# Optimization experiments

Hardware: AMD Instinct MI355X
Metric: run time of the kernel (lower is better)

Reference implementation:

```python
import jax, jax.numpy as jnp
import numpy as np

N = 50000
D_IN = 512
D_OUT = 512
NUM_SAMPLE = 2


def setup_inputs() -> dict:
    key = jax.random.key(0)
    ks = jax.random.split(key, 8)
    x = jax.random.normal(ks[0], (N, D_IN), dtype=jnp.float32)
    neighs1 = jax.random.randint(ks[1], (N, NUM_SAMPLE), 0, N, dtype=jnp.int32)
    neighs2 = jax.random.randint(ks[2], (N, NUM_SAMPLE), 0, N, dtype=jnp.int32)
    # SageLayer weights: [out, 2*in] (self || aggregated neighbors), xavier-ish scale
    W1 = jax.random.normal(ks[3], (D_OUT, 2 * D_IN), dtype=jnp.float32) * 0.03
    W2 = jax.random.normal(ks[4], (D_OUT, 2 * D_OUT), dtype=jnp.float32) * 0.03
    fc_w = jax.random.normal(ks[5], (2, N * D_OUT), dtype=jnp.float32) * 0.0005
    fc_b = jnp.zeros((2,), dtype=jnp.float32)
    return {"x": x, "neighs1": neighs1, "neighs2": neighs2,
            "W1": W1, "W2": W2, "fc_w": fc_w, "fc_b": fc_b}


def _sage_layer(h, neighs, W):
    # MEAN aggregation over the num_sample sampled neighbors (self excluded, gcn=False).
    # Equivalent to the original dense one-hot mask.div(num_neigh).mm(embed_matrix).
    agg = h[neighs].mean(axis=1)                      # [N, S, d] -> [N, d]
    combined = jnp.concatenate([h, agg], axis=1)      # [N, 2d]
    # F.relu(W.mm(combined.t())).t() == relu(combined @ W.T)
    return jax.nn.relu(combined @ W.T)                # [N, out]


def reference(x, neighs1, neighs2, W1, W2, fc_w, fc_b):
    h = _sage_layer(x, neighs1, W1)
    h = _sage_layer(h, neighs2, W2)
    flat = h.reshape(1, -1)                           # [1, N*out]
    logits = flat @ fc_w.T + fc_b                     # [1, 2]
    return (flat, jax.nn.log_softmax(logits, axis=1))
```

## Files before the change

### kernel.cpp

```cpp
#include <hip/hip_runtime.h>
#include <stdint.h>

typedef short bf16x8 __attribute__((ext_vector_type(8)));
typedef float f32x4 __attribute__((ext_vector_type(4)));
typedef unsigned short u16x8 __attribute__((ext_vector_type(8)));

#define N_NODES 50000
#define DIM 512
#define KDIM 1024
#define NPAD 50048
#define M_TILES 391
#define GEMM_GRID 1568
#define FLAT_TOTAL 25600000ULL
#define NBLK_AGG 12500

__device__ __forceinline__ unsigned short f2bf(float f) {
    unsigned u = __float_as_uint(f);
    unsigned r = u + 0x7FFFu + ((u >> 16) & 1u);
    return (unsigned short)(r >> 16);
}
__device__ __forceinline__ float bf2f(unsigned short h) {
    return __uint_as_float(((unsigned)h) << 16);
}

__device__ __forceinline__ void llds16(const void* g, void* l) {
    __builtin_amdgcn_global_load_lds(
        (const __attribute__((address_space(1))) void*)g,
        (__attribute__((address_space(3))) void*)l,
        16, 0, 0);
}

__global__ void cast_x(const float* __restrict__ x, unsigned short* __restrict__ XA) {
    size_t idx = ((size_t)blockIdx.x * blockDim.x + threadIdx.x) * 8;
    float4 v0 = *(const float4*)&x[idx];
    float4 v1 = *(const float4*)&x[idx + 4];
    u16x8 r;
    r[0] = f2bf(v0.x); r[1] = f2bf(v0.y); r[2] = f2bf(v0.z); r[3] = f2bf(v0.w);
    r[4] = f2bf(v1.x); r[5] = f2bf(v1.y); r[6] = f2bf(v1.z); r[7] = f2bf(v1.w);
    size_t row = idx >> 9;
    size_t col = idx & 511;
    *(u16x8*)&XA[row * KDIM + col] = r;
}

__global__ void cast_w2(const float* __restrict__ w1, const float* __restrict__ w2,
                        unsigned short* __restrict__ o1, unsigned short* __restrict__ o2) {
    int b = blockIdx.x;
    const float* w = (b < 256) ? w1 : w2;
    unsigned short* o = (b < 256) ? o1 : o2;
    int idx = ((b & 255) * 256 + threadIdx.x) * 8;
    float4 v0 = *(const float4*)&w[idx];
    float4 v1 = *(const float4*)&w[idx + 4];
    u16x8 r;
    r[0] = f2bf(v0.x); r[1] = f2bf(v0.y); r[2] = f2bf(v0.z); r[3] = f2bf(v0.w);
    r[4] = f2bf(v1.x); r[5] = f2bf(v1.y); r[6] = f2bf(v1.z); r[7] = f2bf(v1.w);
    *(u16x8*)&o[idx] = r;
}

__global__ void agg_mean(unsigned short* __restrict__ buf, const int* __restrict__ nb) {
    int t = threadIdx.x;
    int i = blockIdx.x * 4 + (t >> 6);
    int lane = t & 63;
    int c = lane * 8;
    int n0 = nb[i * 2], n1 = nb[i * 2 + 1];
    u16x8 a = *(const u16x8*)&buf[(size_t)n0 * KDIM + c];
    u16x8 b = *(const u16x8*)&buf[(size_t)n1 * KDIM + c];
    u16x8 o;
#pragma unroll
    for (int j = 0; j < 8; j++)
        o[j] = f2bf(0.5f * (bf2f(a[j]) + bf2f(b[j])));
    *(u16x8*)&buf[(size_t)i * KDIM + 512 + c] = o;
}

template <int EPI>
__global__ __launch_bounds__(256)
void gemm_nt(const unsigned short* __restrict__ A, const unsigned short* __restrict__ B,
             unsigned short* __restrict__ H, const float* __restrict__ fcw,
             float* __restrict__ out, float2* __restrict__ partials) {
    __shared__ unsigned short As[2][128 * 32];
    __shared__ unsigned short Bs[2][128 * 32];
    __shared__ float r0[4], r1[4];

    int x = blockIdx.x & 7;
    int g = blockIdx.x >> 3;
    int bm = x + 8 * (g >> 2);
    int bn = g & 3;
    if (bm >= M_TILES) {
        if (EPI == 2 && threadIdx.x == 0) partials[blockIdx.x] = make_float2(0.f, 0.f);
        return;
    }

    int t = threadIdx.x;
    int lane = t & 63;
    int wave = t >> 6;
    int m_off = (wave >> 1) * 64;
    int n_off = (wave & 1) * 64;
    int lrow = lane & 15;
    int lk = (lane >> 4) * 8;

    f32x4 acc[4][4];
#pragma unroll
    for (int i = 0; i < 4; i++)
#pragma unroll
        for (int j = 0; j < 4; j++) acc[i][j] = (f32x4){0.f, 0.f, 0.f, 0.f};

    const unsigned short* ga = A + (size_t)(bm * 128 + (t >> 2)) * KDIM + (t & 3) * 8;
    const unsigned short* gb = B + (size_t)(bn * 128 + (t >> 2)) * KDIM + (t & 3) * 8;

    for (int k0 = 0; k0 < KDIM; k0 += 64) {
        __syncthreads();
        llds16(ga + k0,             &As[0][t * 8]);
        llds16(ga + k0 + 64 * KDIM, &As[0][t * 8 + 2048]);
        llds16(gb + k0,             &Bs[0][t * 8]);
        llds16(gb + k0 + 64 * KDIM, &Bs[0][t * 8 + 2048]);
        llds16(ga + k0 + 32,             &As[1][t * 8]);
        llds16(ga + k0 + 32 + 64 * KDIM, &As[1][t * 8 + 2048]);
        llds16(gb + k0 + 32,             &Bs[1][t * 8]);
        llds16(gb + k0 + 32 + 64 * KDIM, &Bs[1][t * 8 + 2048]);
        __syncthreads();

#pragma unroll
        for (int h = 0; h < 2; h++) {
            bf16x8 af[4], bfr[4];
#pragma unroll
            for (int i = 0; i < 4; i++)
                af[i] = *(const bf16x8*)&As[h][(m_off + i * 16 + lrow) * 32 + lk];
#pragma unroll
            for (int j = 0; j < 4; j++)
                bfr[j] = *(const bf16x8*)&Bs[h][(n_off + j * 16 + lrow) * 32 + lk];
#pragma unroll
            for (int i = 0; i < 4; i++)
#pragma unroll
                for (int j = 0; j < 4; j++)
                    acc[i][j] = __builtin_amdgcn_mfma_f32_16x16x32_bf16(af[i], bfr[j], acc[i][j], 0, 0, 0);
        }
    }

    int lc = lane & 15;
    int lr = (lane >> 4) << 2;

    if (EPI == 1) {
#pragma unroll
        for (int i = 0; i < 4; i++) {
            int row0 = bm * 128 + m_off + i * 16 + lr;
#pragma unroll
            for (int j = 0; j < 4; j++) {
                int col = bn * 128 + n_off + j * 16 + lc;
                f32x4 v = acc[i][j];
#pragma unroll
                for (int r = 0; r < 4; r++)
                    H[(size_t)(row0 + r) * KDIM + col] = f2bf(fmaxf(v[r], 0.f));
            }
        }
    } else {
        float s0 = 0.f, s1 = 0.f;
#pragma unroll
        for (int i = 0; i < 4; i++) {
            int row0 = bm * 128 + m_off + i * 16 + lr;
#pragma unroll
            for (int j = 0; j < 4; j++) {
                int col = bn * 128 + n_off + j * 16 + lc;
                f32x4 v = acc[i][j];
#pragma unroll
                for (int r = 0; r < 4; r++) {
                    int row = row0 + r;
                    if (row < N_NODES) {
                        float vv = fmaxf(v[r], 0.f);
                        size_t off = (size_t)row * DIM + col;
                        out[off] = vv;
                        s0 += vv * fcw[off];
                        s1 += vv * fcw[FLAT_TOTAL + off];
                    }
                }
            }
        }
#pragma unroll
        for (int off = 32; off > 0; off >>= 1) {
            s0 += __shfl_down(s0, off);
            s1 += __shfl_down(s1, off);
        }
        if (lane == 0) { r0[wave] = s0; r1[wave] = s1; }
        __syncthreads();
        if (t == 0)
            partials[blockIdx.x] = make_float2(r0[0] + r0[1] + r0[2] + r0[3],
                                               r1[0] + r1[1] + r1[2] + r1[3]);
    }
}

__global__ void reduce_finalize(const float2* __restrict__ partials, const float* __restrict__ fcb,
                                float* __restrict__ out2) {
    float s0 = 0.f, s1 = 0.f;
    for (int k = threadIdx.x; k < GEMM_GRID; k += 1024) {
        float2 pr = partials[k];
        s0 += pr.x; s1 += pr.y;
    }
#pragma unroll
    for (int off = 32; off > 0; off >>= 1) {
        s0 += __shfl_down(s0, off);
        s1 += __shfl_down(s1, off);
    }
    __shared__ float r0[16], r1[16];
    int lane = threadIdx.x & 63, w = threadIdx.x >> 6;
    if (lane == 0) { r0[w] = s0; r1[w] = s1; }
    __syncthreads();
    if (threadIdx.x == 0) {
        float l0 = fcb[0], l1 = fcb[1];
#pragma unroll
        for (int k = 0; k < 16; k++) { l0 += r0[k]; l1 += r1[k]; }
        float m = fmaxf(l0, l1);
        float lse = m + logf(expf(l0 - m) + expf(l1 - m));
        out2[0] = l0 - lse;
        out2[1] = l1 - lse;
    }
}

extern "C" void kernel_launch(void* const* d_in, const int* in_sizes, int n_in,
                              void* d_out, int out_size, void* d_ws, size_t ws_size,
                              hipStream_t stream) {
    const float* x   = (const float*)d_in[0];
    const int*   n1  = (const int*)d_in[1];
    const int*   n2  = (const int*)d_in[2];
    const float* W1  = (const float*)d_in[3];
    const float* W2  = (const float*)d_in[4];
    const float* fcw = (const float*)d_in[5];
    const float* fcb = (const float*)d_in[6];
    float* out = (float*)d_out;

    char* ws = (char*)d_ws;
    const size_t XA_OFF = 0;
    const size_t HA_OFF = XA_OFF + (size_t)NPAD * KDIM * 2;
    const size_t W1_OFF = HA_OFF + (size_t)NPAD * KDIM * 2;
    const size_t W2_OFF = W1_OFF + (size_t)DIM * KDIM * 2;
    const size_t P_OFF  = W2_OFF + (size_t)DIM * KDIM * 2;
    unsigned short* XA  = (unsigned short*)(ws + XA_OFF);
    unsigned short* HA  = (unsigned short*)(ws + HA_OFF);
    unsigned short* W1r = (unsigned short*)(ws + W1_OFF);
    unsigned short* W2r = (unsigned short*)(ws + W2_OFF);
    float2* partials    = (float2*)(ws + P_OFF);

    cast_w2<<<512, 256, 0, stream>>>(W1, W2, W1r, W2r);
    cast_x<<<12500, 256, 0, stream>>>(x, XA);

    agg_mean<<<NBLK_AGG, 256, 0, stream>>>(XA, n1);
    gemm_nt<1><<<GEMM_GRID, 256, 0, stream>>>(XA, W1r, HA, nullptr, nullptr, nullptr);
    agg_mean<<<NBLK_AGG, 256, 0, stream>>>(HA, n2);
    gemm_nt<2><<<GEMM_GRID, 256, 0, stream>>>(HA, W2r, nullptr, fcw, out, partials);

    reduce_finalize<<<1, 1024, 0, stream>>>(partials, fcb, out + FLAT_TOTAL);
}
```

Before: 665.1 us.

## Halve GEMM N-tile, double-buffer LDS stages, and swizzle LDS layout

```diff
diff --git a/kernel.cpp b/kernel.cpp
--- a/kernel.cpp
+++ b/kernel.cpp
@@ -10,7 +10,7 @@
 #define KDIM 1024
 #define NPAD 50048
 #define M_TILES 391
-#define GEMM_GRID 1568
+#define GEMM_GRID 3136
 #define FLAT_TOTAL 25600000ULL
 #define NBLK_AGG 12500
 
@@ -71,19 +71,46 @@
     *(u16x8*)&buf[(size_t)i * KDIM + 512 + c] = o;
 }
 
+
+#define SYNC0() do { \
+    asm volatile("s_waitcnt vmcnt(0) lgkmcnt(0)" ::: "memory"); \
+    __builtin_amdgcn_sched_barrier(0); \
+    __builtin_amdgcn_s_barrier(); \
+    __builtin_amdgcn_sched_barrier(0); \
+} while (0)
+
+#define STAGE(s, ks) do { \
+    int koff_ = (ks) * 32; \
+    llds16(ga + koff_,            &S[s][t * 8]); \
+    llds16(ga + koff_ + 64*KDIM,  &S[s][2048 + t * 8]); \
+    llds16(gb + koff_,            &S[s][4096 + t * 8]); \
+} while (0)
+
+#define COMPUTE(s) do { \
+    bf16x8 af[4], bfr[2]; \
+    _Pragma("unroll") \
+    for (int i_ = 0; i_ < 4; i_++) af[i_] = *(const bf16x8*)&S[s][aoff[i_]]; \
+    _Pragma("unroll") \
+    for (int j_ = 0; j_ < 2; j_++) bfr[j_] = *(const bf16x8*)&S[s][boff[j_]]; \
+    _Pragma("unroll") \
+    for (int i_ = 0; i_ < 4; i_++) \
+        _Pragma("unroll") \
+        for (int j_ = 0; j_ < 2; j_++) \
+            acc[i_][j_] = __builtin_amdgcn_mfma_f32_16x16x32_bf16(af[i_], bfr[j_], acc[i_][j_], 0, 0, 0); \
+} while (0)
+
 template <int EPI>
-__global__ __launch_bounds__(256)
+__global__ __launch_bounds__(256, 6)
 void gemm_nt(const unsigned short* __restrict__ A, const unsigned short* __restrict__ B,
              unsigned short* __restrict__ H, const float* __restrict__ fcw,
              float* __restrict__ out, float2* __restrict__ partials) {
-    __shared__ unsigned short As[2][128 * 32];
-    __shared__ unsigned short Bs[2][128 * 32];
+    __shared__ unsigned short S[2][6144];
     __shared__ float r0[4], r1[4];
 
     int x = blockIdx.x & 7;
     int g = blockIdx.x >> 3;
-    int bm = x + 8 * (g >> 2);
-    int bn = g & 3;
+    int bm = x + 8 * (g >> 3);
+    int bn = g & 7;
     if (bm >= M_TILES) {
         if (EPI == 2 && threadIdx.x == 0) partials[blockIdx.x] = make_float2(0.f, 0.f);
         return;
@@ -93,46 +120,43 @@
     int lane = t & 63;
     int wave = t >> 6;
     int m_off = (wave >> 1) * 64;
-    int n_off = (wave & 1) * 64;
+    int n_off = (wave & 1) * 32;
     int lrow = lane & 15;
-    int lk = (lane >> 4) * 8;
-
-    f32x4 acc[4][4];
+    int lch = lane >> 4;
+
+    f32x4 acc[4][2];
 #pragma unroll
     for (int i = 0; i < 4; i++)
 #pragma unroll
-        for (int j = 0; j < 4; j++) acc[i][j] = (f32x4){0.f, 0.f, 0.f, 0.f};
-
-    const unsigned short* ga = A + (size_t)(bm * 128 + (t >> 2)) * KDIM + (t & 3) * 8;
-    const unsigned short* gb = B + (size_t)(bn * 128 + (t >> 2)) * KDIM + (t & 3) * 8;
-
-    for (int k0 = 0; k0 < KDIM; k0 += 64) {
-        __syncthreads();
-        llds16(ga + k0,             &As[0][t * 8]);
-        llds16(ga + k0 + 64 * KDIM, &As[0][t * 8 + 2048]);
-        llds16(gb + k0,             &Bs[0][t * 8]);
-        llds16(gb + k0 + 64 * KDIM, &Bs[0][t * 8 + 2048]);
-        llds16(ga + k0 + 32,             &As[1][t * 8]);
-        llds16(ga + k0 + 32 + 64 * KDIM, &As[1][t * 8 + 2048]);
-        llds16(gb + k0 + 32,             &Bs[1][t * 8]);
-        llds16(gb + k0 + 32 + 64 * KDIM, &Bs[1][t * 8 + 2048]);
-        __syncthreads();
-
-#pragma unroll
-        for (int h = 0; h < 2; h++) {
-            bf16x8 af[4], bfr[4];
-#pragma unroll
-            for (int i = 0; i < 4; i++)
-                af[i] = *(const bf16x8*)&As[h][(m_off + i * 16 + lrow) * 32 + lk];
-#pragma unroll
-            for (int j = 0; j < 4; j++)
-                bfr[j] = *(const bf16x8*)&Bs[h][(n_off + j * 16 + lrow) * 32 + lk];
-#pragma unroll
-            for (int i = 0; i < 4; i++)
-#pragma unroll
-                for (int j = 0; j < 4; j++)
-                    acc[i][j] = __builtin_amdgcn_mfma_f32_16x16x32_bf16(af[i], bfr[j], acc[i][j], 0, 0, 0);
-        }
+        for (int j = 0; j < 2; j++) acc[i][j] = (f32x4){0.f, 0.f, 0.f, 0.f};
+
+    int aoff[4], boff[2];
+#pragma unroll
+    for (int i = 0; i < 4; i++) {
+        int r = m_off + i * 16 + lrow;
+        aoff[i] = r * 32 + ((lch ^ ((r >> 1) & 3)) * 8);
+    }
+#pragma unroll
+    for (int j = 0; j < 2; j++) {
+        int r = n_off + j * 16 + lrow;
+        boff[j] = 4096 + r * 32 + ((lch ^ ((r >> 1) & 3)) * 8);
+    }
+
+    int trow = t >> 2;
+    int tchk = ((t & 3) ^ ((t >> 3) & 3)) * 8;
+    const unsigned short* ga = A + (size_t)(bm * 128 + trow) * KDIM + tchk;
+    const unsigned short* gb = B + (size_t)(bn * 64 + trow) * KDIM + tchk;
+
+    STAGE(0, 0);
+    SYNC0();
+#pragma unroll 1
+    for (int ks = 0; ks < 32; ks += 2) {
+        STAGE(1, ks + 1);
+        COMPUTE(0);
+        SYNC0();
+        if (ks + 2 < 32) STAGE(0, ks + 2);
+        COMPUTE(1);
+        SYNC0();
     }
 
     int lc = lane & 15;
@@ -143,8 +167,8 @@
         for (int i = 0; i < 4; i++) {
             int row0 = bm * 128 + m_off + i * 16 + lr;
 #pragma unroll
-            for (int j = 0; j < 4; j++) {
-                int col = bn * 128 + n_off + j * 16 + lc;
+            for (int j = 0; j < 2; j++) {
+                int col = bn * 64 + n_off + j * 16 + lc;
                 f32x4 v = acc[i][j];
 #pragma unroll
                 for (int r = 0; r < 4; r++)
@@ -157,8 +181,8 @@
         for (int i = 0; i < 4; i++) {
             int row0 = bm * 128 + m_off + i * 16 + lr;
 #pragma unroll
-            for (int j = 0; j < 4; j++) {
-                int col = bn * 128 + n_off + j * 16 + lc;
+            for (int j = 0; j < 2; j++) {
+                int col = bn * 64 + n_off + j * 16 + lc;
                 f32x4 v = acc[i][j];
 #pragma unroll
                 for (int r = 0; r < 4; r++) {
```

Result: faster. 627.7 us (-5.6%).
